# Performance work log

Hardware: AMD Instinct MI355X
Metric: run time of the kernel (lower is better)

The kernel has to match this reference:

```python
import jax, jax.numpy as jnp
import numpy as np

B, C, L = 8, 512, 8192
H = 8  # head_count
DK = C // H  # head key channels
DV = C // H  # head value channels


def setup_inputs() -> dict:
    key = jax.random.key(0)
    ks = jax.random.split(key, 10)
    s = 1.0 / np.sqrt(C)
    return {
        "input_": jax.random.normal(ks[0], (B, C, L), jnp.float32),
        "context_": jax.random.normal(ks[1], (B, C, L), jnp.float32),
        "Wk": jax.random.normal(ks[2], (C, C), jnp.float32) * s,
        "bk": jax.random.normal(ks[3], (C,), jnp.float32) * 0.01,
        "Wq": jax.random.normal(ks[4], (C, C), jnp.float32) * s,
        "bq": jax.random.normal(ks[5], (C,), jnp.float32) * 0.01,
        "Wv": jax.random.normal(ks[6], (C, C), jnp.float32) * s,
        "bv": jax.random.normal(ks[7], (C,), jnp.float32) * 0.01,
        "Wr": jax.random.normal(ks[8], (C, C), jnp.float32) * s,
        "br": jax.random.normal(ks[9], (C,), jnp.float32) * 0.01,
    }


def _proj(W, b, x):
    # 1x1 Conv1d == channel matmul: [O,C] x [B,C,L] -> [B,O,L]
    return jnp.einsum('oc,bcl->bol', W, x) + b[None, :, None]


def reference(input_, context_, Wk, bk, Wq, bq, Wv, bv, Wr, br):
    b, _, l = input_.shape
    keys = _proj(Wk, bk, context_).reshape(b, H, DK, l)
    queries = _proj(Wq, bq, input_).reshape(b, H, DK, l)
    values = _proj(Wv, bv, context_).reshape(b, H, DV, l)
    # per-head: softmax(K) over sequence, softmax(Q) over head-key channels
    k = jax.nn.softmax(keys, axis=3)
    q = jax.nn.softmax(queries, axis=2)
    # context = K @ V^T : [b,h,dk,dv]
    ctx = jnp.einsum('bhkl,bhvl->bhkv', k, values)
    # attended = context^T @ Q : [b,h,dv,l]
    att = jnp.einsum('bhkv,bhkl->bhvl', ctx, q).reshape(b, H * DV, l)
    return _proj(Wr, br, att) + input_
```

## Files before the change

### kernel.cpp

```cpp
#include <hip/hip_runtime.h>

#define NB 8
#define NC 512
#define NL 8192
#define NH 8
#define ND 64

typedef float f32x4 __attribute__((ext_vector_type(4)));
typedef __bf16 bf16x8 __attribute__((ext_vector_type(8)));
typedef unsigned int u32x4 __attribute__((ext_vector_type(4)));

__device__ __forceinline__ unsigned short f2bf(float f) {
    unsigned u = __builtin_bit_cast(unsigned, f);
    u += 0x7fffu + ((u >> 16) & 1u);
    return (unsigned short)(u >> 16);
}
__device__ __forceinline__ bf16x8 frag_from_u32x4(u32x4 v) {
    return __builtin_bit_cast(bf16x8, v);
}
__device__ __forceinline__ bf16x8 ld_frag_lds(const unsigned short* p) {
    const unsigned* q = (const unsigned*)p;
    u32x4 v = { q[0], q[1], q[2], q[3] };
    return frag_from_u32x4(v);
}
__device__ __forceinline__ bf16x8 ld_frag_g16(const unsigned short* p) {
    return frag_from_u32x4(*(const u32x4*)p);
}

__device__ __forceinline__ void gload16(const unsigned short* g, unsigned short* l) {
    __builtin_amdgcn_global_load_lds(
        (const __attribute__((address_space(1))) unsigned int*)g,
        (__attribute__((address_space(3))) unsigned int*)l, 16, 0, 0);
}

__global__ __launch_bounds__(256) void prep_kernel(
    const float* __restrict__ Wk, const float* __restrict__ Wv,
    const float* __restrict__ Wq, const float* __restrict__ Wr,
    const float* __restrict__ bk, const float* __restrict__ bv,
    unsigned short* __restrict__ Wb,
    float* __restrict__ bkv,
    float* __restrict__ zf)
{
    const int WN = NC * NC;
    int i = blockIdx.x * 256 + threadIdx.x;
    if (i < 4 * WN) {
        const float* src = (i < WN) ? Wk : (i < 2 * WN) ? Wv : (i < 3 * WN) ? Wq : Wr;
        Wb[i] = f2bf(src[i & (WN - 1)]);
    } else if (i < 4 * WN + 2 * NC) {
        int j = i - 4 * WN;
        bkv[j] = (j < NC) ? bk[j] : bv[j - NC];
    } else {
        zf[i - (4 * WN + 2 * NC)] = 0.f;
    }
}

__device__ __forceinline__ int ltidx(int c, int l) {
    return c * 64 + ((((l) >> 2) ^ ((c >> 2) & 15)) << 2) + (l & 3);
}
__global__ __launch_bounds__(256) void transpose_cvt_kernel(
    const float* __restrict__ X0, const float* __restrict__ X1,
    unsigned short* __restrict__ Y0, unsigned short* __restrict__ Y1)
{
    const int bz = blockIdx.z;
    const float* X = (bz < NB) ? X0 : X1;
    unsigned short* Y = (bz < NB) ? Y0 : Y1;
    const int b = bz & (NB - 1);
    const int l0 = blockIdx.x * 64, c0 = blockIdx.y * 64;
    const int t = threadIdx.x;
    __shared__ alignas(16) unsigned short lt[64 * 64];
    const float* Xb = X + (size_t)b * NC * NL;
    #pragma unroll
    for (int it = 0; it < 4; ++it) {
        const int c = it * 16 + (t >> 4), l4 = (t & 15) * 4;
        f32x4 v = *(const f32x4*)(Xb + (size_t)(c0 + c) * NL + l0 + l4);
        unsigned lo = f2bf(v.x) | ((unsigned)f2bf(v.y) << 16);
        unsigned hi = f2bf(v.z) | ((unsigned)f2bf(v.w) << 16);
        unsigned* p = (unsigned*)&lt[ltidx(c, l4)];
        p[0] = lo; p[1] = hi;
    }
    __syncthreads();
    unsigned short* Yb = Y + (size_t)b * NL * NC;
    #pragma unroll
    for (int it = 0; it < 2; ++it) {
        const int l = it * 32 + (t >> 3), c8 = (t & 7) * 8;
        u32x4 o;
        #pragma unroll
        for (int d = 0; d < 4; ++d) {
            unsigned lo = lt[ltidx(c8 + 2 * d, l)];
            unsigned hi = lt[ltidx(c8 + 2 * d + 1, l)];
            o[d] = lo | (hi << 16);
        }
        *(u32x4*)(Yb + (size_t)(l0 + l) * NC + c0 + c8) = o;
    }
}

template<int MT, bool RESID, bool PERB, bool QSMT, bool EXPK>
__global__ __launch_bounds__(256) void gemm_kernel(
    const unsigned short* __restrict__ Wb,
    const unsigned short* __restrict__ Xt,
    const float* __restrict__ bias,
    const float* __restrict__ resid,
    void* __restrict__ Yv,
    float* __restrict__ rowsum)
{
    const int bx = blockIdx.x;
    const int g  = bx >> 3;
    const int mt = g % MT;
    const int nt = (g / MT) * 8 + (bx & 7);
    const int b  = blockIdx.y;
    const int t  = threadIdx.x;
    const int wave = t >> 6, lane = t & 63;
    const int m0 = mt * 128, n0 = nt * 128;
    const int wm = (wave & 1) * 64, wn = (wave >> 1) * 64;
    const int OC = MT * 128;

    __shared__ alignas(16) unsigned short lA[128 * 64];
    __shared__ alignas(16) unsigned short lX[128 * 64];

    f32x4 acc[4][4] = {};

    const unsigned short* Wp = Wb + (PERB ? (size_t)b * NC * NC : 0);
    const unsigned short* Xb = Xt + (size_t)b * NL * NC;

    const int lr = lane & 15, q = lane >> 4;
    const unsigned abase = (unsigned)((wm + lr) * 128);
    const unsigned bbase = (unsigned)((wn + lr) * 128);
    const unsigned sw = (unsigned)(lr & 7);

    for (int k0 = 0; k0 < NC; k0 += 64) {
        #pragma unroll
        for (int cc = 0; cc < 4; ++cc) {
            const int pb = wave * 256 + cc * 64;
            const int p  = pb + lane;
            const int r  = p >> 3;
            const int qq = (p & 7) ^ (r & 7);
            gload16(Wp + (size_t)(m0 + r) * NC + k0 + qq * 8, &lA[pb * 8]);
            gload16(Xb + (size_t)(n0 + r) * NC + k0 + qq * 8, &lX[pb * 8]);
        }
        __syncthreads();

        #pragma unroll
        for (int kk = 0; kk < 2; ++kk) {
            const unsigned cq = (((unsigned)(kk * 4 + q)) ^ sw) * 16;
            bf16x8 af[4], bfx[4];
            #pragma unroll
            for (int i = 0; i < 4; ++i)
                af[i] = frag_from_u32x4(*(const u32x4*)((const char*)lA + abase + i * 2048 + cq));
            #pragma unroll
            for (int j = 0; j < 4; ++j)
                bfx[j] = frag_from_u32x4(*(const u32x4*)((const char*)lX + bbase + j * 2048 + cq));
            #pragma unroll
            for (int i = 0; i < 4; ++i)
                #pragma unroll
                for (int j = 0; j < 4; ++j)
                    acc[i][j] = __builtin_amdgcn_mfma_f32_16x16x32_bf16(af[i], bfx[j], acc[i][j], 0, 0, 0);
        }
        __syncthreads();
    }

    const int col = lane & 15, row0 = (lane >> 4) * 4;

    if constexpr (QSMT) {
        #pragma unroll
        for (int i = 0; i < 4; ++i)
            #pragma unroll
            for (int r = 0; r < 4; ++r) {
                const float bo = bias[m0 + wm + i * 16 + row0 + r];
                #pragma unroll
                for (int j = 0; j < 4; ++j) acc[i][j][r] += bo;
            }
        float inv[4];
        #pragma unroll
        for (int j = 0; j < 4; ++j) {
            float m = -1e30f;
            #pragma unroll
            for (int i = 0; i < 4; ++i)
                #pragma unroll
                for (int r = 0; r < 4; ++r) m = fmaxf(m, acc[i][j][r]);
            m = fmaxf(m, __shfl_xor(m, 16));
            m = fmaxf(m, __shfl_xor(m, 32));
            float s = 0.f;
            #pragma unroll
            for (int i = 0; i < 4; ++i)
                #pragma unroll
                for (int r = 0; r < 4; ++r) {
                    const float e = __expf(acc[i][j][r] - m);
                    acc[i][j][r] = e;
                    s += e;
                }
            s += __shfl_xor(s, 16);
            s += __shfl_xor(s, 32);
            inv[j] = 1.0f / s;
        }
        unsigned short* Yq = (unsigned short*)Yv;
        #pragma unroll
        for (int j = 0; j < 4; ++j) {
            const size_t rowb = (size_t)b * NL * NC + (size_t)(n0 + wn + j * 16 + col) * NC;
            #pragma unroll
            for (int i = 0; i < 4; ++i) {
                const int o0 = m0 + wm + i * 16 + row0;
                unsigned lo = f2bf(acc[i][j][0] * inv[j]) | ((unsigned)f2bf(acc[i][j][1] * inv[j]) << 16);
                unsigned hi = f2bf(acc[i][j][2] * inv[j]) | ((unsigned)f2bf(acc[i][j][3] * inv[j]) << 16);
                *(unsigned long long*)(Yq + rowb + o0) =
                    (unsigned long long)lo | ((unsigned long long)hi << 32);
            }
        }
    } else if constexpr (EXPK) {
        unsigned short* Y = (unsigned short*)Yv;
        if (m0 < NC) {
            #pragma unroll
            for (int i = 0; i < 4; ++i)
                #pragma unroll
                for (int r = 0; r < 4; ++r) {
                    const int o = m0 + wm + i * 16 + row0 + r;
                    const float bo = bias[o];
                    const size_t rb = (size_t)b * OC * NL + (size_t)o * NL + n0 + wn;
                    float ps = 0.f;
                    #pragma unroll
                    for (int j = 0; j < 4; ++j) {
                        const float e = __expf(acc[i][j][r] + bo);
                        ps += e;
                        Y[rb + j * 16 + col] = f2bf(e);
                    }
                    #pragma unroll
                    for (int off = 1; off < 16; off <<= 1) ps += __shfl_xor(ps, off);
                    if (col == 0) atomicAdd(&rowsum[(size_t)b * NC + o], ps);
                }
        } else {
            #pragma unroll
            for (int i = 0; i < 4; ++i)
                #pragma unroll
                for (int r = 0; r < 4; ++r) {
                    const int o = m0 + wm + i * 16 + row0 + r;
                    const float bo = bias[o];
                    const size_t rb = (size_t)b * OC * NL + (size_t)o * NL + n0 + wn;
                    #pragma unroll
                    for (int j = 0; j < 4; ++j)
                        Y[rb + j * 16 + col] = f2bf(acc[i][j][r] + bo);
                }
        }
    } else {
        #pragma unroll
        for (int i = 0; i < 4; ++i) {
            #pragma unroll
            for (int r = 0; r < 4; ++r) {
                const int o = m0 + wm + i * 16 + row0 + r;
                const float bo = bias[o];
                const size_t rb = (size_t)b * OC * NL + (size_t)o * NL + n0 + wn;
                if constexpr (RESID) {
                    float* Y = (float*)Yv;
                    #pragma unroll
                    for (int j = 0; j < 4; ++j) {
                        const size_t idx = rb + j * 16 + col;
                        Y[idx] = acc[i][j][r] + bo + resid[idx];
                    }
                } else {
                    unsigned short* Y = (unsigned short*)Yv;
                    #pragma unroll
                    for (int j = 0; j < 4; ++j)
                        Y[rb + j * 16 + col] = f2bf(acc[i][j][r] + bo);
                }
            }
        }
    }
}

__global__ __launch_bounds__(256) void ctx_kernel(
    const unsigned short* __restrict__ KV,
    float* __restrict__ ctx)
{
    const int bh = blockIdx.x;
    const int sp = blockIdx.y;
    const int t = threadIdx.x;
    const int wave = t >> 6, lane = t & 63;
    const int b = bh >> 3, h = bh & 7;
    const size_t base_k = ((size_t)b * 2 * NC + h * ND) * NL;
    const size_t base_v = base_k + (size_t)NC * NL;
    const int i = wave * 16 + (lane & 15);
    const int koff = (lane >> 4) * 8;
    const unsigned short* Ka = KV + base_k + (size_t)i * NL + koff;

    f32x4 acc[4] = {};
    const int l0 = sp * (NL / 16);
    for (int l = l0; l < l0 + (NL / 16); l += 32) {
        bf16x8 a = ld_frag_g16(Ka + l);
        #pragma unroll
        for (int j = 0; j < 4; ++j) {
            bf16x8 bv = ld_frag_g16(KV + base_v + (size_t)(j * 16 + (lane & 15)) * NL + l + koff);
            acc[j] = __builtin_amdgcn_mfma_f32_16x16x32_bf16(a, bv, acc[j], 0, 0, 0);
        }
    }
    const int col = lane & 15, row0 = (lane >> 4) * 4;
    #pragma unroll
    for (int j = 0; j < 4; ++j)
        #pragma unroll
        for (int r = 0; r < 4; ++r)
            atomicAdd(&ctx[(size_t)bh * (ND * ND) + (size_t)(wave * 16 + row0 + r) * ND + j * 16 + col],
                      acc[j][r]);
}

__global__ __launch_bounds__(512) void fold_kernel(
    const unsigned short* __restrict__ Wrb,
    const float* __restrict__ ctxb,
    const float* __restrict__ rowsum,
    unsigned short* __restrict__ Mb)
{
    const int bh = blockIdx.x;
    const int b = bh >> 3, h = bh & 7;
    const int t = threadIdx.x;
    const int wave = t >> 6, lane = t & 63;

    __shared__ unsigned short lc[64 * 66];
    const float* cs = ctxb + (size_t)bh * (ND * ND);
    const float* rs = rowsum + (size_t)b * NC + h * ND;
    #pragma unroll
    for (int it = 0; it < 8; ++it) {
        int i = it * 512 + t;
        lc[(i >> 6) * 66 + (i & 63)] = f2bf(cs[i] / rs[i >> 6]);
    }
    __syncthreads();

    const int koff = (lane >> 4) * 8;
    f32x4 acc[4][4] = {};
    #pragma unroll
    for (int kk = 0; kk < 64; kk += 32) {
        bf16x8 af[4], bfx[4];
        #pragma unroll
        for (int i = 0; i < 4; ++i)
            af[i] = ld_frag_g16(Wrb + (size_t)(wave * 64 + i * 16 + (lane & 15)) * NC
                                + h * ND + kk + koff);
        #pragma unroll
        for (int j = 0; j < 4; ++j)
            bfx[j] = ld_frag_lds(&lc[(j * 16 + (lane & 15)) * 66 + kk + koff]);
        #pragma unroll
        for (int i = 0; i < 4; ++i)
            #pragma unroll
            for (int j = 0; j < 4; ++j)
                acc[i][j] = __builtin_amdgcn_mfma_f32_16x16x32_bf16(af[i], bfx[j], acc[i][j], 0, 0, 0);
    }

    const int col = lane & 15, row0 = (lane >> 4) * 4;
    #pragma unroll
    for (int i = 0; i < 4; ++i)
        #pragma unroll
        for (int r = 0; r < 4; ++r) {
            const int o = wave * 64 + i * 16 + row0 + r;
            #pragma unroll
            for (int j = 0; j < 4; ++j)
                Mb[(size_t)b * NC * NC + (size_t)o * NC + h * ND + j * 16 + col]
                    = f2bf(acc[i][j][r]);
        }
}

extern "C" void kernel_launch(void* const* d_in, const int* in_sizes, int n_in,
                              void* d_out, int out_size, void* d_ws, size_t ws_size,
                              hipStream_t stream) {
    (void)in_sizes; (void)n_in; (void)out_size; (void)ws_size;
    const float* input_   = (const float*)d_in[0];
    const float* context_ = (const float*)d_in[1];
    const float* Wk = (const float*)d_in[2];
    const float* bk = (const float*)d_in[3];
    const float* Wq = (const float*)d_in[4];
    const float* bq = (const float*)d_in[5];
    const float* Wv = (const float*)d_in[6];
    const float* bv = (const float*)d_in[7];
    const float* Wr = (const float*)d_in[8];
    const float* br = (const float*)d_in[9];
    float* out = (float*)d_out;

    char* ws = (char*)d_ws;
    unsigned short* Wkvb = (unsigned short*)ws;
    unsigned short* Wqb  = Wkvb + 2 * NC * NC;
    unsigned short* Wrb  = Wqb + NC * NC;
    float* bkv  = (float*)(Wrb + NC * NC);
    float* ctxb = bkv + 2 * NC;
    float* rowsum = ctxb + NB * NH * ND * ND;
    unsigned short* KVp = (unsigned short*)(rowsum + NB * NC);
    unsigned short* R2  = KVp + (size_t)NB * 2 * NC * NL;
    unsigned short* Mb  = KVp;
    unsigned short* Xt_in = (unsigned short*)d_out;

    const int WN = NC * NC;
    const int prep_elems = 4 * WN + 2 * NC + (NB * NH * ND * ND + NB * NC);
    prep_kernel<<<(prep_elems + 255) / 256, 256, 0, stream>>>(
        Wk, Wv, Wq, Wr, bk, bv, Wkvb, bkv, ctxb);

    transpose_cvt_kernel<<<dim3(NL / 64, NC / 64, 2 * NB), 256, 0, stream>>>(
        context_, input_, R2, Xt_in);

    gemm_kernel<8, false, false, false, true><<<dim3(64 * 8, NB), 256, 0, stream>>>(
        Wkvb, R2, bkv, nullptr, KVp, rowsum);

    gemm_kernel<4, false, false, true, false><<<dim3(64 * 4, NB), 256, 0, stream>>>(
        Wqb, Xt_in, bq, nullptr, R2, nullptr);

    ctx_kernel<<<dim3(NB * NH, 16), 256, 0, stream>>>(KVp, ctxb);
    fold_kernel<<<NB * NH, 512, 0, stream>>>(Wrb, ctxb, rowsum, Mb);

    gemm_kernel<4, true, true, false, false><<<dim3(64 * 4, NB), 256, 0, stream>>>(
        Mb, R2, br, input_, out, nullptr);
}
```

Measured before the change: 707.7 us.

## Fuse weight prep into transpose, halve GEMM K-tile, move K row-sums into ctx MFMA

Weight conversion and zeroing now run in an extra z-slice of the transpose kernel, removing one launch. The GEMM K-step drops from 64 to 32 with a new LDS swizzle, halving shared memory per block to raise occupancy, at the cost of twice as many barriers. The softmax row-sum of exp(K) is no longer built with shuffles and atomics in the KV GEMM epilogue. Instead it comes from an extra MFMA against a ones vector in ctx_kernel, so it now sums the bf16-rounded values.

```diff
diff --git a/kernel.cpp b/kernel.cpp
--- a/kernel.cpp
+++ b/kernel.cpp
@@ -33,16 +33,13 @@
         (__attribute__((address_space(3))) unsigned int*)l, 16, 0, 0);
 }
 
-__global__ __launch_bounds__(256) void prep_kernel(
+__device__ __forceinline__ void prep_body(int i,
     const float* __restrict__ Wk, const float* __restrict__ Wv,
     const float* __restrict__ Wq, const float* __restrict__ Wr,
     const float* __restrict__ bk, const float* __restrict__ bv,
-    unsigned short* __restrict__ Wb,
-    float* __restrict__ bkv,
-    float* __restrict__ zf)
+    unsigned short* __restrict__ Wb, float* __restrict__ bkv, float* __restrict__ zf)
 {
     const int WN = NC * NC;
-    int i = blockIdx.x * 256 + threadIdx.x;
     if (i < 4 * WN) {
         const float* src = (i < WN) ? Wk : (i < 2 * WN) ? Wv : (i < 3 * WN) ? Wq : Wr;
         Wb[i] = f2bf(src[i & (WN - 1)]);
@@ -57,16 +54,27 @@
 __device__ __forceinline__ int ltidx(int c, int l) {
     return c * 64 + ((((l) >> 2) ^ ((c >> 2) & 15)) << 2) + (l & 3);
 }
-__global__ __launch_bounds__(256) void transpose_cvt_kernel(
+__global__ __launch_bounds__(256) void transpose_prep_kernel(
     const float* __restrict__ X0, const float* __restrict__ X1,
-    unsigned short* __restrict__ Y0, unsigned short* __restrict__ Y1)
+    unsigned short* __restrict__ Y0, unsigned short* __restrict__ Y1,
+    const float* __restrict__ Wk, const float* __restrict__ Wv,
+    const float* __restrict__ Wq, const float* __restrict__ Wr,
+    const float* __restrict__ bk, const float* __restrict__ bv,
+    unsigned short* __restrict__ Wb, float* __restrict__ bkv, float* __restrict__ zf)
 {
     const int bz = blockIdx.z;
+    const int t = threadIdx.x;
+    if (bz == 2 * NB) {
+        constexpr int total = 4 * NC * NC + 2 * NC + (NB * NH * ND * ND + NB * NC);
+        const int stride = (NL / 64) * (NC / 64) * 256;
+        for (int i = (blockIdx.y * (NL / 64) + blockIdx.x) * 256 + t; i < total; i += stride)
+            prep_body(i, Wk, Wv, Wq, Wr, bk, bv, Wb, bkv, zf);
+        return;
+    }
     const float* X = (bz < NB) ? X0 : X1;
     unsigned short* Y = (bz < NB) ? Y0 : Y1;
     const int b = bz & (NB - 1);
     const int l0 = blockIdx.x * 64, c0 = blockIdx.y * 64;
-    const int t = threadIdx.x;
     __shared__ alignas(16) unsigned short lt[64 * 64];
     const float* Xb = X + (size_t)b * NC * NL;
     #pragma unroll
@@ -100,8 +108,7 @@
     const unsigned short* __restrict__ Xt,
     const float* __restrict__ bias,
     const float* __restrict__ resid,
-    void* __restrict__ Yv,
-    float* __restrict__ rowsum)
+    void* __restrict__ Yv)
 {
     const int bx = blockIdx.x;
     const int g  = bx >> 3;
@@ -114,8 +121,8 @@
     const int wm = (wave & 1) * 64, wn = (wave >> 1) * 64;
     const int OC = MT * 128;
 
-    __shared__ alignas(16) unsigned short lA[128 * 64];
-    __shared__ alignas(16) unsigned short lX[128 * 64];
+    __shared__ alignas(16) unsigned short lA[128 * 32];
+    __shared__ alignas(16) unsigned short lX[128 * 32];
 
     f32x4 acc[4][4] = {};
 
@@ -123,38 +130,34 @@
     const unsigned short* Xb = Xt + (size_t)b * NL * NC;
 
     const int lr = lane & 15, q = lane >> 4;
-    const unsigned abase = (unsigned)((wm + lr) * 128);
-    const unsigned bbase = (unsigned)((wn + lr) * 128);
-    const unsigned sw = (unsigned)(lr & 7);
-
-    for (int k0 = 0; k0 < NC; k0 += 64) {
-        #pragma unroll
-        for (int cc = 0; cc < 4; ++cc) {
-            const int pb = wave * 256 + cc * 64;
+    const unsigned aoff = (unsigned)((wm + lr) * 64 + (q ^ (((wm + lr) >> 1) & 3)) * 16);
+    const unsigned boff = (unsigned)((wn + lr) * 64 + (q ^ (((wn + lr) >> 1) & 3)) * 16);
+    const int pb0 = wave * 128;
+
+    for (int k0 = 0; k0 < NC; k0 += 32) {
+        #pragma unroll
+        for (int cc = 0; cc < 2; ++cc) {
+            const int pb = pb0 + cc * 64;
             const int p  = pb + lane;
-            const int r  = p >> 3;
-            const int qq = (p & 7) ^ (r & 7);
+            const int r  = p >> 2;
+            const int qq = (p & 3) ^ ((r >> 1) & 3);
             gload16(Wp + (size_t)(m0 + r) * NC + k0 + qq * 8, &lA[pb * 8]);
             gload16(Xb + (size_t)(n0 + r) * NC + k0 + qq * 8, &lX[pb * 8]);
         }
         __syncthreads();
 
-        #pragma unroll
-        for (int kk = 0; kk < 2; ++kk) {
-            const unsigned cq = (((unsigned)(kk * 4 + q)) ^ sw) * 16;
-            bf16x8 af[4], bfx[4];
-            #pragma unroll
-            for (int i = 0; i < 4; ++i)
-                af[i] = frag_from_u32x4(*(const u32x4*)((const char*)lA + abase + i * 2048 + cq));
+        bf16x8 af[4], bfx[4];
+        #pragma unroll
+        for (int i = 0; i < 4; ++i)
+            af[i] = frag_from_u32x4(*(const u32x4*)((const char*)lA + aoff + i * 1024));
+        #pragma unroll
+        for (int j = 0; j < 4; ++j)
+            bfx[j] = frag_from_u32x4(*(const u32x4*)((const char*)lX + boff + j * 1024));
+        #pragma unroll
+        for (int i = 0; i < 4; ++i)
             #pragma unroll
             for (int j = 0; j < 4; ++j)
-                bfx[j] = frag_from_u32x4(*(const u32x4*)((const char*)lX + bbase + j * 2048 + cq));
-            #pragma unroll
-            for (int i = 0; i < 4; ++i)
-                #pragma unroll
-                for (int j = 0; j < 4; ++j)
-                    acc[i][j] = __builtin_amdgcn_mfma_f32_16x16x32_bf16(af[i], bfx[j], acc[i][j], 0, 0, 0);
-        }
+                acc[i][j] = __builtin_amdgcn_mfma_f32_16x16x32_bf16(af[i], bfx[j], acc[i][j], 0, 0, 0);
         __syncthreads();
     }
 
@@ -215,16 +218,9 @@
                     const int o = m0 + wm + i * 16 + row0 + r;
                     const float bo = bias[o];
                     const size_t rb = (size_t)b * OC * NL + (size_t)o * NL + n0 + wn;
-                    float ps = 0.f;
                     #pragma unroll
-                    for (int j = 0; j < 4; ++j) {
-                        const float e = __expf(acc[i][j][r] + bo);
-                        ps += e;
-                        Y[rb + j * 16 + col] = f2bf(e);
-                    }
-                    #pragma unroll
-                    for (int off = 1; off < 16; off <<= 1) ps += __shfl_xor(ps, off);
-                    if (col == 0) atomicAdd(&rowsum[(size_t)b * NC + o], ps);
+                    for (int j = 0; j < 4; ++j)
+                        Y[rb + j * 16 + col] = f2bf(__expf(acc[i][j][r] + bo));
                 }
         } else {
             #pragma unroll
@@ -267,7 +263,8 @@
 
 __global__ __launch_bounds__(256) void ctx_kernel(
     const unsigned short* __restrict__ KV,
-    float* __restrict__ ctx)
+    float* __restrict__ ctx,
+    float* __restrict__ rowsum)
 {
     const int bh = blockIdx.x;
     const int sp = blockIdx.y;
@@ -280,7 +277,11 @@
     const int koff = (lane >> 4) * 8;
     const unsigned short* Ka = KV + base_k + (size_t)i * NL + koff;
 
+    const u32x4 onesw = { 0x3f803f80u, 0x3f803f80u, 0x3f803f80u, 0x3f803f80u };
+    const bf16x8 onef = frag_from_u32x4(onesw);
+
     f32x4 acc[4] = {};
+    f32x4 accs = {};
     const int l0 = sp * (NL / 16);
     for (int l = l0; l < l0 + (NL / 16); l += 32) {
         bf16x8 a = ld_frag_g16(Ka + l);
@@ -289,6 +290,7 @@
             bf16x8 bv = ld_frag_g16(KV + base_v + (size_t)(j * 16 + (lane & 15)) * NL + l + koff);
             acc[j] = __builtin_amdgcn_mfma_f32_16x16x32_bf16(a, bv, acc[j], 0, 0, 0);
         }
+        accs = __builtin_amdgcn_mfma_f32_16x16x32_bf16(a, onef, accs, 0, 0, 0);
     }
     const int col = lane & 15, row0 = (lane >> 4) * 4;
     #pragma unroll
@@ -297,6 +299,11 @@
         for (int r = 0; r < 4; ++r)
             atomicAdd(&ctx[(size_t)bh * (ND * ND) + (size_t)(wave * 16 + row0 + r) * ND + j * 16 + col],
                       acc[j][r]);
+    if (col == 0) {
+        #pragma unroll
+        for (int r = 0; r < 4; ++r)
+            atomicAdd(&rowsum[(size_t)b * NC + h * ND + wave * 16 + row0 + r], accs[r]);
+    }
 }
 
 __global__ __launch_bounds__(512) void fold_kernel(
@@ -380,23 +387,19 @@
     unsigned short* Mb  = KVp;
     unsigned short* Xt_in = (unsigned short*)d_out;
 
-    const int WN = NC * NC;
-    const int prep_elems = 4 * WN + 2 * NC + (NB * NH * ND * ND + NB * NC);
-    prep_kernel<<<(prep_elems + 255) / 256, 256, 0, stream>>>(
+    transpose_prep_kernel<<<dim3(NL / 64, NC / 64, 2 * NB + 1), 256, 0, stream>>>(
+        context_, input_, R2, Xt_in,
         Wk, Wv, Wq, Wr, bk, bv, Wkvb, bkv, ctxb);
 
-    transpose_cvt_kernel<<<dim3(NL / 64, NC / 64, 2 * NB), 256, 0, stream>>>(
-        context_, input_, R2, Xt_in);
-
     gemm_kernel<8, false, false, false, true><<<dim3(64 * 8, NB), 256, 0, stream>>>(
-        Wkvb, R2, bkv, nullptr, KVp, rowsum);
+        Wkvb, R2, bkv, nullptr, KVp);
 
     gemm_kernel<4, false, false, true, false><<<dim3(64 * 4, NB), 256, 0, stream>>>(
-        Wqb, Xt_in, bq, nullptr, R2, nullptr);
-
-    ctx_kernel<<<dim3(NB * NH, 16), 256, 0, stream>>>(KVp, ctxb);
+        Wqb, Xt_in, bq, nullptr, R2);
+
+    ctx_kernel<<<dim3(NB * NH, 16), 256, 0, stream>>>(KVp, ctxb, rowsum);
     fold_kernel<<<NB * NH, 512, 0, stream>>>(Wrb, ctxb, rowsum, Mb);
 
     gemm_kernel<4, true, true, false, false><<<dim3(64 * 4, NB), 256, 0, stream>>>(
-        Mb, R2, br, input_, out, nullptr);
-}
+        Mb, R2, br, input_, out);
+}
```

After: 675.1 us. 1.05x faster.
